# Optimization experiments

Hardware: AMD Instinct MI355X
Metric: run time of the kernel (lower is better)

Reference implementation:

```python
import jax, jax.numpy as jnp
import numpy as np

EMBED = 1024
HEADS = 16
HEAD_DIM = EMBED // HEADS


def setup_inputs() -> dict:
    key = jax.random.key(0)
    ks = jax.random.split(key, 7)
    s = 1.0 / np.sqrt(EMBED)
    return {
        "hidden_states": jax.random.normal(ks[0], (8, 1024, EMBED), dtype=jnp.float32),
        "w_q": jax.random.uniform(ks[1], (EMBED, EMBED), jnp.float32, -s, s),
        "b_q": jax.random.uniform(ks[2], (EMBED,), jnp.float32, -s, s),
        "w_k": jax.random.uniform(ks[3], (EMBED, EMBED), jnp.float32, -s, s),
        "b_k": jax.random.uniform(ks[4], (EMBED,), jnp.float32, -s, s),
        "w_v": jax.random.uniform(ks[5], (EMBED, EMBED), jnp.float32, -s, s),
        "b_v": jax.random.uniform(ks[6], (EMBED,), jnp.float32, -s, s),
    }


def reference(hidden_states, w_q, b_q, w_k, b_k, w_v, b_v):
    b, L, c = hidden_states.shape
    h, d = HEADS, HEAD_DIM
    # torch Linear: x @ W.T + b
    q = hidden_states @ w_q.T + b_q
    k = hidden_states @ w_k.T + b_k
    v = hidden_states @ w_v.T + b_v
    # [b, L, h, d] -> [b, h, L, d]
    q = q.reshape(b, L, h, d).transpose(0, 2, 1, 3)
    k = k.reshape(b, L, h, d).transpose(0, 2, 1, 3)
    v = v.reshape(b, L, h, d).transpose(0, 2, 1, 3)
    scores = jnp.einsum("bhqd,bhkd->bhqk", q, k) * (d ** -0.5)
    probs = jax.nn.softmax(scores, axis=-1)
    out = jnp.einsum("bhqk,bhkd->bhqd", probs, v)  # [b, h, L, d]
    # Faithful to original: .view(b, L, -1) on [b,h,L,d] WITHOUT head transpose
    return out.reshape(b, L, h * d)
```

## Files before the change

### kernel.cpp

```cpp
#include <hip/hip_runtime.h>

#define EMBED 1024
#define HEADS 16
#define HDIM  64

typedef __attribute__((ext_vector_type(8))) short bf16x8;
typedef __attribute__((ext_vector_type(8))) _Float16 f16x8;
typedef __attribute__((ext_vector_type(4))) float f32x4;

#define AS1 __attribute__((address_space(1)))
#define AS3 __attribute__((address_space(3)))

#if __has_builtin(__builtin_amdgcn_exp2f)
#define EXP2F(x) __builtin_amdgcn_exp2f(x)
#else
#define EXP2F(x) exp2f(x)
#endif

__device__ __forceinline__ unsigned bf16_rne(float f) {
    unsigned u = __float_as_uint(f);
    return (u + 0x7FFFu + ((u >> 16) & 1u)) >> 16;
}

__global__ __launch_bounds__(256)
void cast_f16(const float* __restrict__ in, short* __restrict__ outh,
              float scale, int n)
{
    int i = (blockIdx.x * 256 + threadIdx.x) * 8;
    if (i >= n) return;
    float4 a = *(const float4*)(in + i);
    float4 b = *(const float4*)(in + i + 4);
    float f[8] = {a.x, a.y, a.z, a.w, b.x, b.y, b.z, b.w};
    union { _Float16 h[8]; uint4 v; } H;
#pragma unroll
    for (int e = 0; e < 8; ++e) H.h[e] = (_Float16)(f[e] * scale);
    *(uint4*)(outh + i) = H.v;
}

#define STAGE_A(buf, h, kt) do {                                              \
    const short* s0_ = baseA + ((h) * 128) * EMBED + (kt) * 64;               \
    short* d_ = &sh[(buf) * 32768 + (h) * 8192 + t * 8];                      \
    __builtin_amdgcn_global_load_lds((const AS1 void*)s0_, (AS3 void*)d_, 16, 0, 0); \
    __builtin_amdgcn_global_load_lds((const AS1 void*)(s0_ + 64 * EMBED), (AS3 void*)(d_ + 4096), 16, 0, 0); \
} while (0)

#define STAGE_B(buf, h, kt) do {                                              \
    const short* s0_ = baseB + ((h) * 32) * EMBED + (kt) * 64;                \
    short* d_ = &sh[(buf) * 32768 + 16384 + (h) * 8192 + t * 8];              \
    __builtin_amdgcn_global_load_lds((const AS1 void*)s0_, (AS3 void*)d_, 16, 0, 0); \
    __builtin_amdgcn_global_load_lds((const AS1 void*)(s0_ + 128 * EMBED), (AS3 void*)(d_ + 4096), 16, 0, 0); \
} while (0)

__global__ __launch_bounds__(512, 2)
void qkv_mfma(const short* __restrict__ Xh, const short* __restrict__ Wh,
              const float* __restrict__ bq, const float* __restrict__ bk,
              const float* __restrict__ bv,
              short* __restrict__ Qb, short* __restrict__ Kb, short* __restrict__ Vn)
{
    __shared__ short sh[65536];

    const int t = threadIdx.x;
    const int lane = t & 63, quad = lane >> 4, l16 = lane & 15;
    const int w = t >> 6, wm = w >> 2, wn = w & 3;

    const int n0 = blockIdx.x * 256;
    const int m0 = blockIdx.y * 256;

    const int r  = t >> 3;
    const int k8 = ((t & 7) ^ (r & 7)) * 8;
    const short* baseA = Xh + (size_t)(m0 + r) * EMBED + k8;
    const short* baseB = Wh + (size_t)(n0 + (r & 31) + (r >> 5) * 64) * EMBED + k8;

    const int xk0 = ((quad * 16)      ^ ((l16 & 7) << 4)) >> 1;
    const int xk1 = ((64 + quad * 16) ^ ((l16 & 7) << 4)) >> 1;
    const int aOff = wm * 8192 + l16 * 64;
    const int bOff = 16384 + wn * 2048 + l16 * 64;

    f32x4 acc[8][4];
#pragma unroll
    for (int i = 0; i < 8; ++i)
#pragma unroll
        for (int j = 0; j < 4; ++j) acc[i][j] = (f32x4){0.f, 0.f, 0.f, 0.f};

    STAGE_B(0, 0, 0);
    STAGE_A(0, 0, 0);
    STAGE_A(0, 1, 0);
    STAGE_B(0, 1, 0);
    asm volatile("s_waitcnt vmcnt(4)" ::: "memory");
    __builtin_amdgcn_s_barrier();

#pragma unroll 1
    for (int i = 0; i < 8; ++i) {
        const int ktb = 2 * i + 1;
        const int ktc = 2 * i + 2;
        const bool more = (i < 7);
#pragma unroll
        for (int p = 0; p < 8; ++p) {
            const int q = p & 3, buf = p >> 2;
            const int miH = (q & 1) * 4, niH = (q >> 1) * 2;

            f16x8 af[4][2], bf[2][2];
#pragma unroll
            for (int mi = 0; mi < 4; ++mi) {
                const int o = buf * 32768 + aOff + (miH + mi) * 1024;
                af[mi][0] = *(const f16x8*)&sh[o + xk0];
                af[mi][1] = *(const f16x8*)&sh[o + xk1];
            }
#pragma unroll
            for (int ni = 0; ni < 2; ++ni) {
                const int nig = niH + ni;
                const int o = buf * 32768 + bOff + (nig & 1) * 1024 + (nig >> 1) * 8192;
                bf[ni][0] = *(const f16x8*)&sh[o + xk0];
                bf[ni][1] = *(const f16x8*)&sh[o + xk1];
            }

            if      (p == 0) STAGE_B(1, 0, ktb);
            else if (p == 1) STAGE_A(1, 0, ktb);
            else if (p == 2) STAGE_A(1, 1, ktb);
            else if (p == 3) STAGE_B(1, 1, ktb);
            else if (more) {
                if      (p == 4) STAGE_B(0, 0, ktc);
                else if (p == 5) STAGE_A(0, 0, ktc);
                else if (p == 6) STAGE_A(0, 1, ktc);
                else             STAGE_B(0, 1, ktc);
            }

            if (p < 4 || more) asm volatile("s_waitcnt vmcnt(4)" ::: "memory");
            else if (p == 4)   asm volatile("s_waitcnt vmcnt(0)" ::: "memory");
            else               asm volatile("" ::: "memory");
            __builtin_amdgcn_s_barrier();

            __builtin_amdgcn_s_setprio(1);
#pragma unroll
            for (int mi = 0; mi < 4; ++mi)
#pragma unroll
                for (int ni = 0; ni < 2; ++ni) {
                    acc[miH + mi][niH + ni] = __builtin_amdgcn_mfma_f32_16x16x32_f16(
                        af[mi][0], bf[ni][0], acc[miH + mi][niH + ni], 0, 0, 0);
                    acc[miH + mi][niH + ni] = __builtin_amdgcn_mfma_f32_16x16x32_f16(
                        af[mi][1], bf[ni][1], acc[miH + mi][niH + ni], 0, 0, 0);
                }
            __builtin_amdgcn_s_setprio(0);
            __builtin_amdgcn_s_barrier();
        }
    }

    const int mat = n0 >> 10;
    const float* bias = (mat == 0) ? bq : (mat == 1) ? bk : bv;
    short* Out = (mat == 0) ? Qb : (mat == 1) ? Kb : Vn;
    const float s = (mat == 0) ? 0.125f * 1.4426950408889634f : 1.0f;
    const float fs = s * (1.0f / 256.0f);
    const int nm0 = n0 & 1023;
    float bias_v[4];
#pragma unroll
    for (int ni = 0; ni < 4; ++ni) bias_v[ni] = bias[nm0 + wn * 64 + ni * 16 + l16] * s;
    const int bidx = m0 >> 10;
    const int l0   = m0 & 1023;

#pragma unroll
    for (int mi = 0; mi < 8; ++mi) {
        __syncthreads();
#pragma unroll
        for (int ni = 0; ni < 4; ++ni) {
            const int col = wn * 64 + ni * 16 + l16;
#pragma unroll
            for (int rr = 0; rr < 4; ++rr) {
                const int srow = wm * 16 + quad * 4 + rr;
                sh[srow * 268 + col] =
                    (short)(unsigned short)bf16_rne(fmaf(acc[mi][ni][rr], fs, bias_v[ni]));
            }
        }
        __syncthreads();
        const int srw = t >> 4;
        const int c0  = (t & 15) * 16;
        uint4 v0 = *(uint4*)&sh[srw * 268 + c0];
        uint4 v1 = *(uint4*)&sh[srw * 268 + c0 + 8];
        const int wmS = srw >> 4, rloc = srw & 15;
        const int l = l0 + wmS * 128 + mi * 16 + rloc;
        const int nm = nm0 + c0;
        const int head = nm >> 6, d0 = nm & 63;
        short* pDst = Out + ((size_t)(bidx * HEADS + head) * 1024 + l) * 64 + d0;
        *(uint4*)pDst = v0;
        *(uint4*)(pDst + 8) = v1;
    }
}

__global__ __launch_bounds__(256)
void vtrans(const short* __restrict__ Vn, short* __restrict__ Vt)
{
    __shared__ int tile[64 * 65];
    const int t  = threadIdx.x;
    const int lt = blockIdx.x;
    const int bh = blockIdx.y;
    const int lq = t >> 3, dc = (t & 7) * 8;
    const short* src = Vn + ((size_t)bh * 1024 + lt * 64) * 64;
#pragma unroll
    for (int h = 0; h < 2; ++h) {
        const int l = lq + h * 32;
        union { uint4 v; unsigned short us[8]; } ld;
        ld.v = *(const uint4*)&src[l * 64 + dc];
#pragma unroll
        for (int j = 0; j < 8; ++j) tile[(dc + j) * 65 + l] = ld.us[j];
    }
    __syncthreads();
    const int dr = t >> 3, lblk = (t & 7) * 8;
    short* dst = Vt + (size_t)bh * 64 * 1024 + lt * 64;
#pragma unroll
    for (int h = 0; h < 2; ++h) {
        const int d = dr + h * 32;
        union { uint4 v; unsigned short us[8]; } o;
#pragma unroll
        for (int j = 0; j < 8; ++j) o.us[j] = (unsigned short)tile[d * 65 + lblk + j];
        *(uint4*)&dst[(size_t)d * 1024 + lblk] = o.v;
    }
}

__global__ __launch_bounds__(256)
void attn_mfma(const short* __restrict__ Qb, const short* __restrict__ Kb,
               const short* __restrict__ Vt, float* __restrict__ out)
{
    __shared__ short smem[20480];

    const int t  = threadIdx.x;
    const int qt = blockIdx.x, h = blockIdx.y, b = blockIdx.z;
    const int bh = b * HEADS + h;
    const int lane = t & 63, quad = lane >> 4, l16 = lane & 15;
    const int w = t >> 6;
    const int srow = t & 63, schunk = t >> 6;

    {
        const short* gq = Qb + ((size_t)bh * 1024 + qt * 64 + srow) * 64 + schunk * 8;
        __builtin_amdgcn_global_load_lds((const AS1 void*)gq,        (AS3 void*)&smem[t * 8],         16, 0, 0);
        __builtin_amdgcn_global_load_lds((const AS1 void*)(gq + 32), (AS3 void*)&smem[(t + 256) * 8], 16, 0, 0);
        const short* gk = Kb + ((size_t)bh * 1024 + srow) * 64 + schunk * 8;
        __builtin_amdgcn_global_load_lds((const AS1 void*)gk,        (AS3 void*)&smem[4096 + t * 8],         16, 0, 0);
        __builtin_amdgcn_global_load_lds((const AS1 void*)(gk + 32), (AS3 void*)&smem[4096 + (t + 256) * 8], 16, 0, 0);
        const short* gv = Vt + ((size_t)bh * 64 + srow) * 1024 + schunk * 8;
        __builtin_amdgcn_global_load_lds((const AS1 void*)gv,        (AS3 void*)&smem[12288 + t * 8],         16, 0, 0);
        __builtin_amdgcn_global_load_lds((const AS1 void*)(gv + 32), (AS3 void*)&smem[12288 + (t + 256) * 8], 16, 0, 0);
    }
    __syncthreads();

    bf16x8 qfrag[2];
#pragma unroll
    for (int kh = 0; kh < 2; ++kh)
        qfrag[kh] = *(const bf16x8*)&smem[((quad + 4 * kh) * 64 + w * 16 + l16) * 8];

    f32x4 O[4];
#pragma unroll
    for (int i = 0; i < 4; ++i) O[i] = (f32x4){0.f, 0.f, 0.f, 0.f};
    float l_i = 0.f;

    for (int kt = 0; kt < 16; ++kt) {
        const int cur = kt & 1, nxt = cur ^ 1;
        if (kt < 15) {
            const short* gk = Kb + ((size_t)bh * 1024 + (kt + 1) * 64 + srow) * 64 + schunk * 8;
            __builtin_amdgcn_global_load_lds((const AS1 void*)gk,        (AS3 void*)&smem[4096 + nxt * 4096 + t * 8],         16, 0, 0);
            __builtin_amdgcn_global_load_lds((const AS1 void*)(gk + 32), (AS3 void*)&smem[4096 + nxt * 4096 + (t + 256) * 8], 16, 0, 0);
            const short* gv = Vt + ((size_t)bh * 64 + srow) * 1024 + (kt + 1) * 64 + schunk * 8;
            __builtin_amdgcn_global_load_lds((const AS1 void*)gv,        (AS3 void*)&smem[12288 + nxt * 4096 + t * 8],         16, 0, 0);
            __builtin_amdgcn_global_load_lds((const AS1 void*)(gv + 32), (AS3 void*)&smem[12288 + nxt * 4096 + (t + 256) * 8], 16, 0, 0);
        }

        const short* Kc = &smem[4096 + cur * 4096];
        const short* Vc = &smem[12288 + cur * 4096];

        f32x4 ST[4];
#pragma unroll
        for (int mi = 0; mi < 4; ++mi) ST[mi] = (f32x4){0.f, 0.f, 0.f, 0.f};
#pragma unroll
        for (int kh = 0; kh < 2; ++kh)
#pragma unroll
            for (int mi = 0; mi < 4; ++mi) {
                const bf16x8 ka = *(const bf16x8*)&Kc[((quad + 4 * kh) * 64 + mi * 16 + l16) * 8];
                ST[mi] = __builtin_amdgcn_mfma_f32_16x16x32_bf16(ka, qfrag[kh], ST[mi], 0, 0, 0);
            }

        float p[4][4];
        float rs = 0.f;
#pragma unroll
        for (int mi = 0; mi < 4; ++mi)
#pragma unroll
            for (int rr = 0; rr < 4; ++rr) { p[mi][rr] = EXP2F(ST[mi][rr]); rs += p[mi][rr]; }
        l_i += rs;

        unsigned pk[4][2];
#pragma unroll
        for (int mi = 0; mi < 4; ++mi) {
            pk[mi][0] = bf16_rne(p[mi][0]) | (bf16_rne(p[mi][1]) << 16);
            pk[mi][1] = bf16_rne(p[mi][2]) | (bf16_rne(p[mi][3]) << 16);
        }
        const int srcA = (quad & 1) * 32 + l16;
        const int srcB = srcA + 16;
        const bool hi = quad >= 2;
        union { unsigned u[4]; bf16x8 v; } pa[2];
        {
            unsigned a00 = __shfl((int)pk[0][0], srcA), a10 = __shfl((int)pk[1][0], srcA);
            unsigned a01 = __shfl((int)pk[0][1], srcA), a11 = __shfl((int)pk[1][1], srcA);
            unsigned b00 = __shfl((int)pk[0][0], srcB), b10 = __shfl((int)pk[1][0], srcB);
            unsigned b01 = __shfl((int)pk[0][1], srcB), b11 = __shfl((int)pk[1][1], srcB);
            pa[0].u[0] = hi ? a10 : a00;  pa[0].u[1] = hi ? a11 : a01;
            pa[0].u[2] = hi ? b10 : b00;  pa[0].u[3] = hi ? b11 : b01;
            unsigned c00 = __shfl((int)pk[2][0], srcA), c10 = __shfl((int)pk[3][0], srcA);
            unsigned c01 = __shfl((int)pk[2][1], srcA), c11 = __shfl((int)pk[3][1], srcA);
            unsigned d00 = __shfl((int)pk[2][0], srcB), d10 = __shfl((int)pk[3][0], srcB);
            unsigned d01 = __shfl((int)pk[2][1], srcB), d11 = __shfl((int)pk[3][1], srcB);
            pa[1].u[0] = hi ? c10 : c00;  pa[1].u[1] = hi ? c11 : c01;
            pa[1].u[2] = hi ? d10 : d00;  pa[1].u[3] = hi ? d11 : d01;
        }

#pragma unroll
        for (int kh = 0; kh < 2; ++kh)
#pragma unroll
            for (int mi = 0; mi < 4; ++mi) {
                const bf16x8 va = *(const bf16x8*)&Vc[((quad + 4 * kh) * 64 + mi * 16 + l16) * 8];
                O[mi] = __builtin_amdgcn_mfma_f32_16x16x32_bf16(va, pa[kh].v, O[mi], 0, 0, 0);
            }

        __syncthreads();
    }

    l_i += __shfl_xor(l_i, 16);
    l_i += __shfl_xor(l_i, 32);

    float* Os = (float*)&smem[4096];
    const float inv = 1.0f / l_i;
#pragma unroll
    for (int mi = 0; mi < 4; ++mi) {
        f32x4 v;
#pragma unroll
        for (int rr = 0; rr < 4; ++rr) v[rr] = O[mi][rr] * inv;
        *(f32x4*)&Os[(w * 16 + l16) * 68 + mi * 16 + quad * 4] = v;
    }
    __syncthreads();
    {
        const int q = t >> 2, dbase = (t & 3) * 16;
        float* op = out + ((size_t)bh * 1024 + qt * 64 + q) * 64 + dbase;
#pragma unroll
        for (int i = 0; i < 4; ++i)
            *(float4*)&op[i * 4] = *(float4*)&Os[q * 68 + dbase + i * 4];
    }
}

extern "C" void kernel_launch(void* const* d_in, const int* in_sizes, int n_in,
                              void* d_out, int out_size, void* d_ws, size_t ws_size,
                              hipStream_t stream)
{
    const float* X  = (const float*)d_in[0];
    const float* Wq = (const float*)d_in[1];
    const float* bq = (const float*)d_in[2];
    const float* Wk = (const float*)d_in[3];
    const float* bk = (const float*)d_in[4];
    const float* Wv = (const float*)d_in[5];
    const float* bv = (const float*)d_in[6];
    float* out = (float*)d_out;

    const size_t per = (size_t)8 * HEADS * 1024 * HDIM;
    short* Qb = (short*)d_ws;
    short* Kb = Qb + per;
    short* Vt = Kb + per;
    short* Xh = Vt + per;
    short* Wh = Xh + per;
    short* Vn = (short*)d_out;

    const int nX = (int)per;
    const int nW = 1048576;

    cast_f16<<<nX / (8 * 256), 256, 0, stream>>>(X,  Xh,          1.0f,   nX);
    cast_f16<<<nW / (8 * 256), 256, 0, stream>>>(Wq, Wh,          256.0f, nW);
    cast_f16<<<nW / (8 * 256), 256, 0, stream>>>(Wk, Wh + nW,     256.0f, nW);
    cast_f16<<<nW / (8 * 256), 256, 0, stream>>>(Wv, Wh + 2 * nW, 256.0f, nW);

    qkv_mfma<<<dim3(12, 32), 512, 0, stream>>>(Xh, Wh, bq, bk, bv, Qb, Kb, Vn);
    vtrans<<<dim3(16, 128), 256, 0, stream>>>(Vn, Vt);
    attn_mfma<<<dim3(16, HEADS, 8), 256, 0, stream>>>(Qb, Kb, Vt, out);
}
```

Before: 253.7 us.

## Permute K rows on load so P fragments need no cross-lane shuffles

K tile rows are loaded into LDS in a permuted order, so the S^T accumulator layout from the first MFMA already matches the B-operand layout the PV MFMA needs. This removes the sixteen ds_bpermute shuffles and selects per iteration, and packs P to bf16 with the hardware v_cvt_pk_bf16_f32 instead of a manual round-to-nearest-even. It also raises wave priority around the MFMA blocks with s_setprio. The gain depends on the row permutation being exactly right; an error would silently break correctness.

```diff
diff --git a/kernel.cpp b/kernel.cpp
--- a/kernel.cpp
+++ b/kernel.cpp
@@ -228,11 +228,14 @@
     const int w = t >> 6;
     const int srow = t & 63, schunk = t >> 6;
 
+    const int prow = ((srow >> 4) & 1) * 32 + ((srow >> 2) & 3) * 8
+                   + (srow >> 5) * 4 + (srow & 3);
+
     {
         const short* gq = Qb + ((size_t)bh * 1024 + qt * 64 + srow) * 64 + schunk * 8;
         __builtin_amdgcn_global_load_lds((const AS1 void*)gq,        (AS3 void*)&smem[t * 8],         16, 0, 0);
         __builtin_amdgcn_global_load_lds((const AS1 void*)(gq + 32), (AS3 void*)&smem[(t + 256) * 8], 16, 0, 0);
-        const short* gk = Kb + ((size_t)bh * 1024 + srow) * 64 + schunk * 8;
+        const short* gk = Kb + ((size_t)bh * 1024 + prow) * 64 + schunk * 8;
         __builtin_amdgcn_global_load_lds((const AS1 void*)gk,        (AS3 void*)&smem[4096 + t * 8],         16, 0, 0);
         __builtin_amdgcn_global_load_lds((const AS1 void*)(gk + 32), (AS3 void*)&smem[4096 + (t + 256) * 8], 16, 0, 0);
         const short* gv = Vt + ((size_t)bh * 64 + srow) * 1024 + schunk * 8;
@@ -254,7 +257,7 @@
     for (int kt = 0; kt < 16; ++kt) {
         const int cur = kt & 1, nxt = cur ^ 1;
         if (kt < 15) {
-            const short* gk = Kb + ((size_t)bh * 1024 + (kt + 1) * 64 + srow) * 64 + schunk * 8;
+            const short* gk = Kb + ((size_t)bh * 1024 + (kt + 1) * 64 + prow) * 64 + schunk * 8;
             __builtin_amdgcn_global_load_lds((const AS1 void*)gk,        (AS3 void*)&smem[4096 + nxt * 4096 + t * 8],         16, 0, 0);
             __builtin_amdgcn_global_load_lds((const AS1 void*)(gk + 32), (AS3 void*)&smem[4096 + nxt * 4096 + (t + 256) * 8], 16, 0, 0);
             const short* gv = Vt + ((size_t)bh * 64 + srow) * 1024 + (kt + 1) * 64 + schunk * 8;
@@ -268,6 +271,7 @@
         f32x4 ST[4];
 #pragma unroll
         for (int mi = 0; mi < 4; ++mi) ST[mi] = (f32x4){0.f, 0.f, 0.f, 0.f};
+        __builtin_amdgcn_s_setprio(1);
 #pragma unroll
         for (int kh = 0; kh < 2; ++kh)
 #pragma unroll
@@ -275,6 +279,7 @@
                 const bf16x8 ka = *(const bf16x8*)&Kc[((quad + 4 * kh) * 64 + mi * 16 + l16) * 8];
                 ST[mi] = __builtin_amdgcn_mfma_f32_16x16x32_bf16(ka, qfrag[kh], ST[mi], 0, 0, 0);
             }
+        __builtin_amdgcn_s_setprio(0);
 
         float p[4][4];
         float rs = 0.f;
@@ -284,31 +289,16 @@
             for (int rr = 0; rr < 4; ++rr) { p[mi][rr] = EXP2F(ST[mi][rr]); rs += p[mi][rr]; }
         l_i += rs;
 
-        unsigned pk[4][2];
-#pragma unroll
-        for (int mi = 0; mi < 4; ++mi) {
-            pk[mi][0] = bf16_rne(p[mi][0]) | (bf16_rne(p[mi][1]) << 16);
-            pk[mi][1] = bf16_rne(p[mi][2]) | (bf16_rne(p[mi][3]) << 16);
+        union { unsigned u[4]; bf16x8 v; } pa[2];
+#pragma unroll
+        for (int kh = 0; kh < 2; ++kh) {
+            asm("v_cvt_pk_bf16_f32 %0, %1, %2" : "=v"(pa[kh].u[0]) : "v"(p[kh][0]),     "v"(p[kh][1]));
+            asm("v_cvt_pk_bf16_f32 %0, %1, %2" : "=v"(pa[kh].u[1]) : "v"(p[kh][2]),     "v"(p[kh][3]));
+            asm("v_cvt_pk_bf16_f32 %0, %1, %2" : "=v"(pa[kh].u[2]) : "v"(p[kh + 2][0]), "v"(p[kh + 2][1]));
+            asm("v_cvt_pk_bf16_f32 %0, %1, %2" : "=v"(pa[kh].u[3]) : "v"(p[kh + 2][2]), "v"(p[kh + 2][3]));
         }
-        const int srcA = (quad & 1) * 32 + l16;
-        const int srcB = srcA + 16;
-        const bool hi = quad >= 2;
-        union { unsigned u[4]; bf16x8 v; } pa[2];
-        {
-            unsigned a00 = __shfl((int)pk[0][0], srcA), a10 = __shfl((int)pk[1][0], srcA);
-            unsigned a01 = __shfl((int)pk[0][1], srcA), a11 = __shfl((int)pk[1][1], srcA);
-            unsigned b00 = __shfl((int)pk[0][0], srcB), b10 = __shfl((int)pk[1][0], srcB);
-            unsigned b01 = __shfl((int)pk[0][1], srcB), b11 = __shfl((int)pk[1][1], srcB);
-            pa[0].u[0] = hi ? a10 : a00;  pa[0].u[1] = hi ? a11 : a01;
-            pa[0].u[2] = hi ? b10 : b00;  pa[0].u[3] = hi ? b11 : b01;
-            unsigned c00 = __shfl((int)pk[2][0], srcA), c10 = __shfl((int)pk[3][0], srcA);
-            unsigned c01 = __shfl((int)pk[2][1], srcA), c11 = __shfl((int)pk[3][1], srcA);
-            unsigned d00 = __shfl((int)pk[2][0], srcB), d10 = __shfl((int)pk[3][0], srcB);
-            unsigned d01 = __shfl((int)pk[2][1], srcB), d11 = __shfl((int)pk[3][1], srcB);
-            pa[1].u[0] = hi ? c10 : c00;  pa[1].u[1] = hi ? c11 : c01;
-            pa[1].u[2] = hi ? d10 : d00;  pa[1].u[3] = hi ? d11 : d01;
-        }
-
+
+        __builtin_amdgcn_s_setprio(1);
 #pragma unroll
         for (int kh = 0; kh < 2; ++kh)
 #pragma unroll
@@ -316,6 +306,7 @@
                 const bf16x8 va = *(const bf16x8*)&Vc[((quad + 4 * kh) * 64 + mi * 16 + l16) * 8];
                 O[mi] = __builtin_amdgcn_mfma_f32_16x16x32_bf16(va, pa[kh].v, O[mi], 0, 0, 0);
             }
+        __builtin_amdgcn_s_setprio(0);
 
         __syncthreads();
     }
```

After: 249.7 us. No clear change (-1.6%).
